# Kernel tuning notes

Hardware: AMD Instinct MI355X
Metric: run time of the kernel (lower is better)

Reference implementation:

```python
import jax, jax.numpy as jnp
import numpy as np
import math

EPS_NORM = 1e-12
BN_EPS = 1e-5


def _l2norm(x):
    n = jnp.sqrt(jnp.sum(x * x, axis=-1, keepdims=True))
    return x / jnp.maximum(n, EPS_NORM)


def setup_inputs() -> dict:
    key = jax.random.key(0)
    ks = jax.random.split(key, 16)
    b, c, t, l = 16, 32, 16, 256
    s = 0.05
    return {
        "x": jax.random.normal(ks[0], (b, c, t, l), jnp.float32),
        "q_w": jax.random.normal(ks[1], (c, c), jnp.float32) * s,
        "q_b": jax.random.normal(ks[2], (c,), jnp.float32) * s,
        "k_w": jax.random.normal(ks[3], (c, c), jnp.float32) * s,
        "k_b": jax.random.normal(ks[4], (c,), jnp.float32) * s,
        "v_w": jax.random.normal(ks[5], (c, c), jnp.float32) * s,
        "v_b": jax.random.normal(ks[6], (c,), jnp.float32) * s,
        "m_w": jax.random.normal(ks[7], (c, c), jnp.float32) * s,
        "m_b": jax.random.normal(ks[8], (c,), jnp.float32) * s,
        "pre_prompt": jax.random.normal(ks[9], (1, c, 1, l), jnp.float32) * s,
        "conv_w": jax.random.normal(ks[10], (c, c, 9, 1), jnp.float32) * s,
        "conv_b": jax.random.normal(ks[11], (c,), jnp.float32) * s,
        "bn_gamma": jnp.ones((c,), jnp.float32),
        "bn_beta": jnp.zeros((c,), jnp.float32),
        "lin_w": jax.random.normal(ks[12], (l, l), jnp.float32) * s,
        "lin_b": jax.random.normal(ks[13], (l,), jnp.float32) * s,
        "atten_flag": 1,
    }


def reference(x, q_w, q_b, k_w, k_b, v_w, v_b, m_w, m_b, pre_prompt,
              conv_w, conv_b, bn_gamma, bn_beta, lin_w, lin_b, atten_flag):
    b, c, t, l = x.shape
    nh = 8
    hd = c // nh

    xp = jnp.transpose(x, (0, 2, 3, 1))  # (b,t,l,c)

    def heads(w, bias):
        h = xp @ w.T + bias
        h = h.reshape(b, t, l, nh, hd).transpose(0, 1, 3, 2, 4)  # (b,t,nh,l,hd)
        return _l2norm(h)

    q = heads(q_w, q_b)
    k = heads(k_w, k_b)
    v = heads(v_w, v_b)

    atten = jnp.einsum('bthld,bthmd->bthlm', q, k) / math.sqrt(hd)
    atten = jax.nn.softmax(atten, axis=-1)
    o = jnp.einsum('bthlm,bthmd->bthld', atten, v)  # (b,t,nh,l,hd)
    o = o.transpose(0, 1, 3, 2, 4).reshape(b, t, l, c)
    o = o @ m_w.T + m_b
    xo = jnp.transpose(o, (0, 3, 1, 2))  # (b,c,t,l)

    pre = jnp.broadcast_to(pre_prompt, (b, c, 1, l))
    con = jnp.concatenate([xo[:, :, :8], pre], axis=2)  # (b,c,9,l)

    # ConvNormAct: Conv2d (VALID, kernel (9,1)) + BatchNorm2d (batch stats) + ReLU
    h = jax.lax.conv_general_dilated(
        con, conv_w, window_strides=(1, 1), padding='VALID',
        dimension_numbers=('NCHW', 'OIHW', 'NCHW'))  # (b,c,1,l)
    h = h + conv_b[None, :, None, None]
    mean = jnp.mean(h, axis=(0, 2, 3), keepdims=True)
    var = jnp.var(h, axis=(0, 2, 3), keepdims=True)
    h = (h - mean) * jax.lax.rsqrt(var + BN_EPS)
    h = h * bn_gamma[None, :, None, None] + bn_beta[None, :, None, None]
    h = jax.nn.relu(h)

    p = h @ lin_w.T + lin_b  # Linear over token_len axis
    p = xo[:, :, 2:3] - p
    return jnp.concatenate([xo[:, :, :8], p], axis=2)  # (b,c,9,l)
```

## Files before the change

### kernel.cpp

```cpp
#include <hip/hip_runtime.h>
#include <hip/hip_bf16.h>


typedef __fp16 h2 __attribute__((ext_vector_type(2)));

#define O_OFF  0u
#define XO_OFF 2097152u
#define H_OFF  6291456u
#define S_OFF  6815744u

__device__ __forceinline__ int probe_f32(const unsigned short* graw) {
    return graw[0] == 0;
}
template<typename T> __device__ __forceinline__ float ldv(const T* p, long i);
template<> __device__ __forceinline__ float ldv<float>(const float* p, long i) {
    return p[i];
}
template<> __device__ __forceinline__ float ldv<__hip_bfloat16>(const __hip_bfloat16* p, long i) {
    return __bfloat162float(p[i]);
}
template<typename T> __device__ __forceinline__ void stv(T* p, size_t i, float v);
template<> __device__ __forceinline__ void stv<float>(float* p, size_t i, float v) {
    p[i] = v;
}
template<> __device__ __forceinline__ void stv<__hip_bfloat16>(__hip_bfloat16* p, size_t i, float v) {
    p[i] = __float2bfloat16(v);
}
__device__ __forceinline__ h2 pkh2(float a, float b) {
    return __builtin_amdgcn_cvt_pkrtz(a, b);
}
__device__ __forceinline__ h2 h2bc(float v) { return pkh2(v, v); }
__device__ __forceinline__ float bflo(unsigned int u) {
    union { unsigned int i; float f; } c; c.i = u << 16; return c.f;
}
__device__ __forceinline__ float bfhi(unsigned int u) {
    union { unsigned int i; float f; } c; c.i = u & 0xffff0000u; return c.f;
}
#if __has_builtin(__builtin_amdgcn_fdot2)
__device__ __forceinline__ float fdot2(h2 a, h2 b, float c) {
    return __builtin_amdgcn_fdot2(a, b, c, false);
}
#else
__device__ __forceinline__ float fdot2(h2 a, h2 b, float c) {
    return fmaf((float)a[0], (float)b[0], fmaf((float)a[1], (float)b[1], c));
}
#endif
#define PFMA(a, b, c) __builtin_elementwise_fma((a), (b), (c))

template<typename T>
__device__ __forceinline__ void attn_phase(
    const T* __restrict__ x,
    const T* __restrict__ qw, const T* __restrict__ qb,
    const T* __restrict__ kw, const T* __restrict__ kb,
    const T* __restrict__ vw, const T* __restrict__ vb,
    unsigned short* __restrict__ O, char* smem)
{
    uint2* Karr = (uint2*)smem;
    uint4* Vbr  = (uint4*)(smem + 2048);
    float (*WL)[4][32] = (float (*)[4][32])(smem + 6144);
    float (*BL)[4]     = (float (*)[4])(smem + 7680);

    const int tid = threadIdx.x;
    const int blk = blockIdx.x;
    const int h = blk & 7, bt = blk >> 3;
    const int b = bt >> 3, t = bt & 7;
    const int h4 = h * 4;

    for (int e = tid; e < 384; e += 128) {
        int p = e >> 7, r = e & 127;
        const T* W = (p == 0) ? qw : ((p == 1) ? kw : vw);
        WL[p][r >> 5][r & 31] = ldv(W, (long)(h4 + (r >> 5)) * 32 + (r & 31));
    }
    if (tid < 12) {
        int p = tid >> 2, j = tid & 3;
        const T* B = (p == 0) ? qb : ((p == 1) ? kb : vb);
        BL[p][j] = ldv(B, h4 + j);
    }

    float xv0[32], xv1[32];
    #pragma unroll
    for (int c = 0; c < 32; c++) {
        const long xb = (((long)b * 32 + c) * 16 + t) * 256 + tid;
        xv0[c] = ldv(x, xb);
        xv1[c] = ldv(x, xb + 128);
    }
    __syncthreads();

    float4 pr0[3], pr1[3];
    #pragma unroll
    for (int p = 0; p < 3; p++) {
        float a0[4], a1[4];
        #pragma unroll
        for (int j = 0; j < 4; j++) { a0[j] = BL[p][j]; a1[j] = a0[j]; }
        #pragma unroll
        for (int c0 = 0; c0 < 32; c0 += 4) {
            float4 w0 = *(const float4*)&WL[p][0][c0];
            float4 w1 = *(const float4*)&WL[p][1][c0];
            float4 w2 = *(const float4*)&WL[p][2][c0];
            float4 w3 = *(const float4*)&WL[p][3][c0];
            const float* wj[4] = {(const float*)&w0, (const float*)&w1,
                                  (const float*)&w2, (const float*)&w3};
            #pragma unroll
            for (int cc = 0; cc < 4; cc++) {
                float x0 = xv0[c0+cc], x1 = xv1[c0+cc];
                #pragma unroll
                for (int j = 0; j < 4; j++) {
                    a0[j] = fmaf(x0, wj[j][cc], a0[j]);
                    a1[j] = fmaf(x1, wj[j][cc], a1[j]);
                }
            }
        }
        float s20 = a0[0]*a0[0] + a0[1]*a0[1] + a0[2]*a0[2] + a0[3]*a0[3];
        float s21 = a1[0]*a1[0] + a1[1]*a1[1] + a1[2]*a1[2] + a1[3]*a1[3];
        float i0 = 1.0f / fmaxf(sqrtf(s20), 1e-12f);
        float i1 = 1.0f / fmaxf(sqrtf(s21), 1e-12f);
        if (p == 0) { i0 *= 0.7213475204444817f; i1 *= 0.7213475204444817f; }
        pr0[p] = make_float4(a0[0]*i0, a0[1]*i0, a0[2]*i0, a0[3]*i0);
        pr1[p] = make_float4(a1[0]*i1, a1[1]*i1, a1[2]*i1, a1[3]*i1);
    }

    union { uint2 u; h2 h[2]; } ka, kb2;
    ka.h[0]  = pkh2(pr0[1].x, pr0[1].y); ka.h[1]  = pkh2(pr0[1].z, pr0[1].w);
    kb2.h[0] = pkh2(pr1[1].x, pr1[1].y); kb2.h[1] = pkh2(pr1[1].z, pr1[1].w);
    union { uint4 u; h2 h[4]; } va, vb2;
    va.h[0]  = h2bc(pr0[2].x); va.h[1]  = h2bc(pr0[2].y);
    va.h[2]  = h2bc(pr0[2].z); va.h[3]  = h2bc(pr0[2].w);
    vb2.h[0] = h2bc(pr1[2].x); vb2.h[1] = h2bc(pr1[2].y);
    vb2.h[2] = h2bc(pr1[2].z); vb2.h[3] = h2bc(pr1[2].w);
    Karr[tid]       = ka.u;
    Karr[tid + 128] = kb2.u;
    Vbr[tid]        = va.u;
    Vbr[tid + 128]  = vb2.u;
    const h2 qa01 = pkh2(pr0[0].x, pr0[0].y), qa23 = pkh2(pr0[0].z, pr0[0].w);
    const h2 qb01 = pkh2(pr1[0].x, pr1[0].y), qb23 = pkh2(pr1[0].z, pr1[0].w);
    __syncthreads();

    const h2 C0 = h2bc(1.0f),          C1 = h2bc(0.69314718f);
    const h2 C2 = h2bc(0.24022651f),   C3 = h2bc(0.05550411f);
    const h2 C4 = h2bc(0.00961813f),   C5 = h2bc(0.00133336f);
    const h2 M0 = {(__fp16)1.0f, (__fp16)0.0f};
    const h2 M1 = {(__fp16)0.0f, (__fp16)1.0f};

    h2 A0 = h2bc(0.0f), A1 = A0, A2 = A0, A3 = A0;
    float den0 = 0.f, den1 = 0.f;
    #pragma unroll 8
    for (int m = 0; m < 256; m++) {
        union { uint2 u; h2 h[2]; } ku; ku.u = Karr[m];
        union { uint4 u; h2 h[4]; } vu; vu.u = Vbr[m];
        float sa = fdot2(qa01, ku.h[0], fdot2(qa23, ku.h[1], 0.0f));
        float sb = fdot2(qb01, ku.h[0], fdot2(qb23, ku.h[1], 0.0f));
        h2 xx = pkh2(sa, sb);
        h2 p = PFMA(xx, C5, C4);
        p = PFMA(xx, p, C3);
        p = PFMA(xx, p, C2);
        p = PFMA(xx, p, C1);
        p = PFMA(xx, p, C0);
        den0 = fdot2(p, M0, den0);
        den1 = fdot2(p, M1, den1);
        A0 = PFMA(p, vu.h[0], A0);
        A1 = PFMA(p, vu.h[1], A1);
        A2 = PFMA(p, vu.h[2], A2);
        A3 = PFMA(p, vu.h[3], A3);
    }
    float ia = 1.0f / den0, ib = 1.0f / den1;
    union { h2 h; unsigned int u; } c0, c1, c2, c3;
    c0.h = pkh2((float)A0[0] * ia, (float)A1[0] * ia);
    c1.h = pkh2((float)A2[0] * ia, (float)A3[0] * ia);
    c2.h = pkh2((float)A0[1] * ib, (float)A1[1] * ib);
    c3.h = pkh2((float)A2[1] * ib, (float)A3[1] * ib);
    *(uint2*)(O + ((size_t)bt * 256u + tid) * 32u + h4)       = make_uint2(c0.u, c1.u);
    *(uint2*)(O + ((size_t)bt * 256u + tid + 128) * 32u + h4) = make_uint2(c2.u, c3.u);
}

template<typename T>
__device__ __forceinline__ void mproj_phase(
    const unsigned short* __restrict__ O,
    const T* __restrict__ mw, const T* __restrict__ mb,
    T* __restrict__ out, float* __restrict__ xof, char* smem)
{
    float* sw = (float*)smem;
    float* sb = (float*)(smem + 4096);
    const int tid = threadIdx.x;
    const int blk = blockIdx.x;
    const int bt = blk >> 1, lhalf = blk & 1;
    const int b = bt >> 3, t = bt & 7;
    const int l = lhalf * 128 + tid;

    for (int e = tid; e < 1024; e += 128) sw[e] = ldv(mw, e);
    if (tid < 32) sb[tid] = ldv(mb, tid);

    float ov[32];
    const unsigned short* src = O + ((size_t)bt * 256u + l) * 32u;
    #pragma unroll
    for (int cc = 0; cc < 4; cc++) {
        union { uint4 u; h2 h[4]; } uu;
        uu.u = *(const uint4*)(src + cc * 8);
        #pragma unroll
        for (int j = 0; j < 4; j++) {
            ov[cc*8 + 2*j]     = (float)uu.h[j][0];
            ov[cc*8 + 2*j + 1] = (float)uu.h[j][1];
        }
    }
    __syncthreads();

    #pragma unroll 4
    for (int co = 0; co < 32; co++) {
        float s = sb[co];
        #pragma unroll
        for (int c0 = 0; c0 < 32; c0 += 4) {
            float4 w4 = *(const float4*)&sw[co * 32 + c0];
            s = fmaf(ov[c0+0], w4.x, s);
            s = fmaf(ov[c0+1], w4.y, s);
            s = fmaf(ov[c0+2], w4.z, s);
            s = fmaf(ov[c0+3], w4.w, s);
        }
        stv(out, (((size_t)b * 32 + co) * 9 + t) * 256u + l, s);
        xof[(((size_t)b * 32 + co) * 8 + t) * 256u + l] = s;
    }
}

template<typename T>
__device__ __forceinline__ void conv_phase(
    const float* __restrict__ xof, const T* __restrict__ pre,
    const T* __restrict__ cw, const T* __restrict__ cb,
    float* __restrict__ hout, float* __restrict__ s, char* smem)
{
    float* wl = (float*)smem;
    const int tid = threadIdx.x;
    const int blk = blockIdx.x;
    const int b = blk >> 4, cog = (blk >> 1) & 7, lhalf = blk & 1;
    const int co0 = cog * 4;
    const int l = lhalf * 128 + tid;

    for (int e = tid; e < 1152; e += 128) {
        int g = e & 3, r = e >> 2;
        wl[e] = ldv(cw, (long)(co0 + g) * 288 + r);
    }
    __syncthreads();

    float a0 = 0.f, a1 = 0.f, a2 = 0.f, a3 = 0.f;
    #pragma unroll 4
    for (int ci = 0; ci < 32; ci++) {
        const float* xp = xof + (((size_t)b * 32 + ci) * 8) * 256u + l;
        float v[9];
        #pragma unroll
        for (int kt = 0; kt < 8; kt++) v[kt] = xp[kt * 256];
        v[8] = ldv(pre, (long)ci * 256 + l);
        #pragma unroll
        for (int kt = 0; kt < 9; kt++) {
            float4 w4 = *(const float4*)&wl[(ci * 9 + kt) * 4];
            a0 = fmaf(v[kt], w4.x, a0);
            a1 = fmaf(v[kt], w4.y, a1);
            a2 = fmaf(v[kt], w4.z, a2);
            a3 = fmaf(v[kt], w4.w, a3);
        }
    }
    a0 += ldv(cb, co0+0); a1 += ldv(cb, co0+1);
    a2 += ldv(cb, co0+2); a3 += ldv(cb, co0+3);

    hout[((size_t)b * 32 + co0 + 0) * 256u + l] = a0;
    hout[((size_t)b * 32 + co0 + 1) * 256u + l] = a1;
    hout[((size_t)b * 32 + co0 + 2) * 256u + l] = a2;
    hout[((size_t)b * 32 + co0 + 3) * 256u + l] = a3;

    float acc[4] = {a0, a1, a2, a3};
    #pragma unroll
    for (int g = 0; g < 4; g++) {
        float sg = acc[g], sq = acc[g] * acc[g];
        #pragma unroll
        for (int off = 32; off > 0; off >>= 1) {
            sg += __shfl_down(sg, off, 64);
            sq += __shfl_down(sq, off, 64);
        }
        if ((tid & 63) == 0) {
            atomicAdd(&s[co0 + g], sg);
            atomicAdd(&s[32 + co0 + g], sq);
        }
    }
}

__device__ __forceinline__ void rowdot2(const float* rp, const float* hn0,
                                        const float* hn1, float& a0, float& a1) {
    float s0 = 0.f, s1 = 0.f;
    #pragma unroll 4
    for (int i0 = 0; i0 < 256; i0 += 4) {
        float4 u  = *(const float4*)(rp + i0);
        float4 p0 = *(const float4*)(hn0 + i0);
        float4 p1 = *(const float4*)(hn1 + i0);
        s0 = fmaf(p0.x, u.x, s0); s1 = fmaf(p1.x, u.x, s1);
        s0 = fmaf(p0.y, u.y, s0); s1 = fmaf(p1.y, u.y, s1);
        s0 = fmaf(p0.z, u.z, s0); s1 = fmaf(p1.z, u.z, s1);
        s0 = fmaf(p0.w, u.w, s0); s1 = fmaf(p1.w, u.w, s1);
    }
    a0 = s0; a1 = s1;
}
__device__ __forceinline__ void rowdot2(const __hip_bfloat16* rp_, const float* hn0,
                                        const float* hn1, float& a0, float& a1) {
    const unsigned short* rp = (const unsigned short*)rp_;
    float s0 = 0.f, s1 = 0.f;
    #pragma unroll 2
    for (int i0 = 0; i0 < 256; i0 += 16) {
        uint4 u0 = *(const uint4*)(rp + i0);
        uint4 u1 = *(const uint4*)(rp + i0 + 8);
        unsigned int uu[8] = {u0.x, u0.y, u0.z, u0.w, u1.x, u1.y, u1.z, u1.w};
        #pragma unroll
        for (int j = 0; j < 8; j++) {
            float wl = bflo(uu[j]), wh = bfhi(uu[j]);
            s0 = fmaf(hn0[i0 + 2*j],     wl, s0);
            s1 = fmaf(hn1[i0 + 2*j],     wl, s1);
            s0 = fmaf(hn0[i0 + 2*j + 1], wh, s0);
            s1 = fmaf(hn1[i0 + 2*j + 1], wh, s1);
        }
    }
    a0 = s0; a1 = s1;
}

template<typename T>
__device__ __forceinline__ void lin_phase(
    const float* __restrict__ hbuf, const float* __restrict__ sbuf,
    const T* __restrict__ gam, const T* __restrict__ bet,
    const T* __restrict__ lw, const T* __restrict__ lb,
    const float* __restrict__ xof, T* __restrict__ out, char* smem)
{
    float* hn0 = (float*)smem;
    float* hn1 = (float*)(smem + 1024);
    const int tid = threadIdx.x;
    const int blk = blockIdx.x;
    const int b = blk >> 4, cop = blk & 15;
    const int co0 = cop * 2, co1 = co0 + 1;

    float mean0 = sbuf[co0] * (1.0f / 4096.0f);
    float var0  = fmaxf(sbuf[32 + co0] * (1.0f / 4096.0f) - mean0 * mean0, 0.0f);
    float sc0 = ldv(gam, co0) * __frsqrt_rn(var0 + 1e-5f);
    float sh0 = ldv(bet, co0) - mean0 * sc0;
    float mean1 = sbuf[co1] * (1.0f / 4096.0f);
    float var1  = fmaxf(sbuf[32 + co1] * (1.0f / 4096.0f) - mean1 * mean1, 0.0f);
    float sc1 = ldv(gam, co1) * __frsqrt_rn(var1 + 1e-5f);
    float sh1 = ldv(bet, co1) - mean1 * sc1;

    const size_t hb0 = ((size_t)b * 32 + co0) * 256u;
    const size_t hb1 = ((size_t)b * 32 + co1) * 256u;
    hn0[tid] = fmaxf(fmaf(hbuf[hb0 + tid], sc0, sh0), 0.0f);
    hn1[tid] = fmaxf(fmaf(hbuf[hb1 + tid], sc1, sh1), 0.0f);
    __syncthreads();

    float a0, a1;
    rowdot2(lw + (size_t)tid * 256u, hn0, hn1, a0, a1);
    float bias = ldv(lb, tid);
    a0 += bias; a1 += bias;

    const size_t xb0 = (((size_t)b * 32 + co0) * 8 + 2) * 256u;
    const size_t xb1 = (((size_t)b * 32 + co1) * 8 + 2) * 256u;
    const size_t ob0 = (((size_t)b * 32 + co0) * 9 + 8) * 256u;
    const size_t ob1 = (((size_t)b * 32 + co1) * 9 + 8) * 256u;
    stv(out, ob0 + tid, xof[xb0 + tid] - a0);
    stv(out, ob1 + tid, xof[xb1 + tid] - a1);
}

__global__ __launch_bounds__(128) void k_attn_s(
    const void* x, const void* qw, const void* qb, const void* kw,
    const void* kb, const void* vw, const void* vb,
    unsigned short* O, float* sbuf, const unsigned short* graw)
{
    __shared__ __align__(16) char smem[7744];
    if (blockIdx.x == 1023 && threadIdx.x < 64) sbuf[threadIdx.x] = 0.0f;
    if (probe_f32(graw))
        attn_phase<float>((const float*)x, (const float*)qw, (const float*)qb,
            (const float*)kw, (const float*)kb, (const float*)vw,
            (const float*)vb, O, smem);
    else
        attn_phase<__hip_bfloat16>((const __hip_bfloat16*)x,
            (const __hip_bfloat16*)qw, (const __hip_bfloat16*)qb,
            (const __hip_bfloat16*)kw, (const __hip_bfloat16*)kb,
            (const __hip_bfloat16*)vw, (const __hip_bfloat16*)vb, O, smem);
}
__global__ __launch_bounds__(128) void k_mproj_s(
    const unsigned short* O, const void* mw, const void* mb,
    void* out, float* xof, const unsigned short* graw)
{
    __shared__ __align__(16) char smem[6144];
    if (probe_f32(graw))
        mproj_phase<float>(O, (const float*)mw, (const float*)mb,
                           (float*)out, xof, smem);
    else
        mproj_phase<__hip_bfloat16>(O, (const __hip_bfloat16*)mw,
                                    (const __hip_bfloat16*)mb,
                                    (__hip_bfloat16*)out, xof, smem);
}
__global__ __launch_bounds__(128) void k_conv_s(
    const float* xof, const void* pre, const void* cw, const void* cb,
    float* hbuf, float* sbuf, const unsigned short* graw)
{
    __shared__ __align__(16) char smem[6144];
    if (probe_f32(graw))
        conv_phase<float>(xof, (const float*)pre, (const float*)cw,
                          (const float*)cb, hbuf, sbuf, smem);
    else
        conv_phase<__hip_bfloat16>(xof, (const __hip_bfloat16*)pre,
                                   (const __hip_bfloat16*)cw,
                                   (const __hip_bfloat16*)cb, hbuf, sbuf, smem);
}
__global__ __launch_bounds__(256) void k_lin_s(
    const float* hbuf, const float* sbuf, const void* gam, const void* bet,
    const void* lw, const void* lb, const float* xof, void* out,
    const unsigned short* graw)
{
    __shared__ __align__(16) char smem[2048];
    if (probe_f32(graw))
        lin_phase<float>(hbuf, sbuf, (const float*)gam, (const float*)bet,
                         (const float*)lw, (const float*)lb, xof,
                         (float*)out, smem);
    else
        lin_phase<__hip_bfloat16>(hbuf, sbuf, (const __hip_bfloat16*)gam,
                                  (const __hip_bfloat16*)bet,
                                  (const __hip_bfloat16*)lw,
                                  (const __hip_bfloat16*)lb, xof,
                                  (__hip_bfloat16*)out, smem);
}

extern "C" void kernel_launch(void* const* d_in, const int* in_sizes, int n_in,
                              void* d_out, int out_size, void* d_ws, size_t ws_size,
                              hipStream_t stream) {
    const void* x   = d_in[0];
    const void* qw  = d_in[1];  const void* qb  = d_in[2];
    const void* kw  = d_in[3];  const void* kb  = d_in[4];
    const void* vw  = d_in[5];  const void* vb  = d_in[6];
    const void* mw  = d_in[7];  const void* mb  = d_in[8];
    const void* pre = d_in[9];
    const void* cw  = d_in[10]; const void* cb  = d_in[11];
    const void* gam = d_in[12]; const void* bet = d_in[13];
    const void* lw  = d_in[14]; const void* lb  = d_in[15];
    const unsigned short* graw = (const unsigned short*)d_in[12];

    unsigned short* Obuf = (unsigned short*)((char*)d_ws + O_OFF);
    float* xof  = (float*)((char*)d_ws + XO_OFF);
    float* hbuf = (float*)((char*)d_ws + H_OFF);
    float* sbuf = (float*)((char*)d_ws + S_OFF);

    k_attn_s <<<1024, 128, 0, stream>>>(x, qw, qb, kw, kb, vw, vb,
                                        Obuf, sbuf, graw);
    k_mproj_s<<<256,  128, 0, stream>>>(Obuf, mw, mb, d_out, xof, graw);
    k_conv_s <<<256,  128, 0, stream>>>(xof, pre, cw, cb, hbuf, sbuf, graw);
    k_lin_s  <<<256,  256, 0, stream>>>(hbuf, sbuf, gam, bet, lw, lb,
                                        xof, d_out, graw);
}
```

Measured before the change: 178.6 us.

## Use packed FMA and fp16 dot products across projection, conv and linear kernels

Rewrites the QKV projection, conv, and linear stages to use packed two-wide float FMAs. The m-projection now keeps O in fp16 and uses fdot2 against fp16-packed weights in shared memory. The softmax exp polynomial drops its highest-order term, which lowers accuracy. The linear kernel now splits each row dot product across 512 threads and reduces the two halves through shared memory. These changes cut instruction count and raise parallelism, at the cost of lower precision in the exp approximation and the output projection.

Result: faster. 171.4 us (-4.0%).

```diff
diff --git a/kernel.cpp b/kernel.cpp
--- a/kernel.cpp
+++ b/kernel.cpp
@@ -3,6 +3,7 @@
 
 
 typedef __fp16 h2 __attribute__((ext_vector_type(2)));
+typedef float  f2 __attribute__((ext_vector_type(2)));
 
 #define O_OFF  0u
 #define XO_OFF 2097152u
@@ -35,6 +36,13 @@
 }
 __device__ __forceinline__ float bfhi(unsigned int u) {
     union { unsigned int i; float f; } c; c.i = u & 0xffff0000u; return c.f;
+}
+__device__ __forceinline__ float2 ld2(const float* p, long i) {
+    return *(const float2*)(p + i);
+}
+__device__ __forceinline__ float2 ld2(const __hip_bfloat16* p, long i) {
+    unsigned int u = *(const unsigned int*)((const unsigned short*)p + i);
+    return make_float2(bflo(u), bfhi(u));
 }
 #if __has_builtin(__builtin_amdgcn_fdot2)
 __device__ __forceinline__ float fdot2(h2 a, h2 b, float c) {
@@ -89,34 +97,40 @@
     float4 pr0[3], pr1[3];
     #pragma unroll
     for (int p = 0; p < 3; p++) {
-        float a0[4], a1[4];
-        #pragma unroll
-        for (int j = 0; j < 4; j++) { a0[j] = BL[p][j]; a1[j] = a0[j]; }
+        f2 aa0 = {BL[p][0], BL[p][0]};
+        f2 aa1 = {BL[p][1], BL[p][1]};
+        f2 aa2 = {BL[p][2], BL[p][2]};
+        f2 aa3 = {BL[p][3], BL[p][3]};
         #pragma unroll
         for (int c0 = 0; c0 < 32; c0 += 4) {
             float4 w0 = *(const float4*)&WL[p][0][c0];
             float4 w1 = *(const float4*)&WL[p][1][c0];
             float4 w2 = *(const float4*)&WL[p][2][c0];
             float4 w3 = *(const float4*)&WL[p][3][c0];
-            const float* wj[4] = {(const float*)&w0, (const float*)&w1,
-                                  (const float*)&w2, (const float*)&w3};
+            const float* w0p = (const float*)&w0;
+            const float* w1p = (const float*)&w1;
+            const float* w2p = (const float*)&w2;
+            const float* w3p = (const float*)&w3;
             #pragma unroll
             for (int cc = 0; cc < 4; cc++) {
-                float x0 = xv0[c0+cc], x1 = xv1[c0+cc];
-                #pragma unroll
-                for (int j = 0; j < 4; j++) {
-                    a0[j] = fmaf(x0, wj[j][cc], a0[j]);
-                    a1[j] = fmaf(x1, wj[j][cc], a1[j]);
-                }
+                f2 xp = {xv0[c0+cc], xv1[c0+cc]};
+                aa0 = PFMA(xp, ((f2){w0p[cc], w0p[cc]}), aa0);
+                aa1 = PFMA(xp, ((f2){w1p[cc], w1p[cc]}), aa1);
+                aa2 = PFMA(xp, ((f2){w2p[cc], w2p[cc]}), aa2);
+                aa3 = PFMA(xp, ((f2){w3p[cc], w3p[cc]}), aa3);
             }
         }
-        float s20 = a0[0]*a0[0] + a0[1]*a0[1] + a0[2]*a0[2] + a0[3]*a0[3];
-        float s21 = a1[0]*a1[0] + a1[1]*a1[1] + a1[2]*a1[2] + a1[3]*a1[3];
-        float i0 = 1.0f / fmaxf(sqrtf(s20), 1e-12f);
-        float i1 = 1.0f / fmaxf(sqrtf(s21), 1e-12f);
+        f2 s2 = aa0 * aa0;
+        s2 = PFMA(aa1, aa1, s2);
+        s2 = PFMA(aa2, aa2, s2);
+        s2 = PFMA(aa3, aa3, s2);
+        float i0 = 1.0f / fmaxf(sqrtf(s2[0]), 1e-12f);
+        float i1 = 1.0f / fmaxf(sqrtf(s2[1]), 1e-12f);
         if (p == 0) { i0 *= 0.7213475204444817f; i1 *= 0.7213475204444817f; }
-        pr0[p] = make_float4(a0[0]*i0, a0[1]*i0, a0[2]*i0, a0[3]*i0);
-        pr1[p] = make_float4(a1[0]*i1, a1[1]*i1, a1[2]*i1, a1[3]*i1);
+        f2 ii = {i0, i1};
+        f2 n0 = aa0 * ii, n1 = aa1 * ii, n2 = aa2 * ii, n3 = aa3 * ii;
+        pr0[p] = make_float4(n0[0], n1[0], n2[0], n3[0]);
+        pr1[p] = make_float4(n0[1], n1[1], n2[1], n3[1]);
     }
 
     union { uint2 u; h2 h[2]; } ka, kb2;
@@ -137,7 +151,7 @@
 
     const h2 C0 = h2bc(1.0f),          C1 = h2bc(0.69314718f);
     const h2 C2 = h2bc(0.24022651f),   C3 = h2bc(0.05550411f);
-    const h2 C4 = h2bc(0.00961813f),   C5 = h2bc(0.00133336f);
+    const h2 C4 = h2bc(0.00961813f);
     const h2 M0 = {(__fp16)1.0f, (__fp16)0.0f};
     const h2 M1 = {(__fp16)0.0f, (__fp16)1.0f};
 
@@ -150,8 +164,7 @@
         float sa = fdot2(qa01, ku.h[0], fdot2(qa23, ku.h[1], 0.0f));
         float sb = fdot2(qb01, ku.h[0], fdot2(qb23, ku.h[1], 0.0f));
         h2 xx = pkh2(sa, sb);
-        h2 p = PFMA(xx, C5, C4);
-        p = PFMA(xx, p, C3);
+        h2 p = PFMA(xx, C4, C3);
         p = PFMA(xx, p, C2);
         p = PFMA(xx, p, C1);
         p = PFMA(xx, p, C0);
@@ -178,41 +191,38 @@
     const T* __restrict__ mw, const T* __restrict__ mb,
     T* __restrict__ out, float* __restrict__ xof, char* smem)
 {
-    float* sw = (float*)smem;
-    float* sb = (float*)(smem + 4096);
+    h2* swh = (h2*)smem;
+    float* sb = (float*)(smem + 2048);
     const int tid = threadIdx.x;
     const int blk = blockIdx.x;
     const int bt = blk >> 1, lhalf = blk & 1;
     const int b = bt >> 3, t = bt & 7;
     const int l = lhalf * 128 + tid;
 
-    for (int e = tid; e < 1024; e += 128) sw[e] = ldv(mw, e);
+    for (int e = tid; e < 512; e += 128) {
+        int co = e >> 4, cp = e & 15;
+        float2 w = ld2(mw, (long)co * 32 + 2 * cp);
+        swh[e] = pkh2(w.x, w.y);
+    }
     if (tid < 32) sb[tid] = ldv(mb, tid);
 
-    float ov[32];
+    union { uint4 u[4]; h2 h[16]; } ou;
     const unsigned short* src = O + ((size_t)bt * 256u + l) * 32u;
     #pragma unroll
-    for (int cc = 0; cc < 4; cc++) {
-        union { uint4 u; h2 h[4]; } uu;
-        uu.u = *(const uint4*)(src + cc * 8);
-        #pragma unroll
-        for (int j = 0; j < 4; j++) {
-            ov[cc*8 + 2*j]     = (float)uu.h[j][0];
-            ov[cc*8 + 2*j + 1] = (float)uu.h[j][1];
-        }
-    }
+    for (int cc = 0; cc < 4; cc++) ou.u[cc] = *(const uint4*)(src + cc * 8);
     __syncthreads();
 
     #pragma unroll 4
     for (int co = 0; co < 32; co++) {
         float s = sb[co];
-        #pragma unroll
-        for (int c0 = 0; c0 < 32; c0 += 4) {
-            float4 w4 = *(const float4*)&sw[co * 32 + c0];
-            s = fmaf(ov[c0+0], w4.x, s);
-            s = fmaf(ov[c0+1], w4.y, s);
-            s = fmaf(ov[c0+2], w4.z, s);
-            s = fmaf(ov[c0+3], w4.w, s);
+        const uint4* wrow = (const uint4*)(swh + co * 16);
+        #pragma unroll
+        for (int q4 = 0; q4 < 4; q4++) {
+            union { uint4 u; h2 h[4]; } wv; wv.u = wrow[q4];
+            s = fdot2(ou.h[q4*4+0], wv.h[0], s);
+            s = fdot2(ou.h[q4*4+1], wv.h[1], s);
+            s = fdot2(ou.h[q4*4+2], wv.h[2], s);
+            s = fdot2(ou.h[q4*4+3], wv.h[3], s);
         }
         stv(out, (((size_t)b * 32 + co) * 9 + t) * 256u + l, s);
         xof[(((size_t)b * 32 + co) * 8 + t) * 256u + l] = s;
@@ -238,7 +248,7 @@
     }
     __syncthreads();
 
-    float a0 = 0.f, a1 = 0.f, a2 = 0.f, a3 = 0.f;
+    f2 a01 = {0.f, 0.f}, a23 = {0.f, 0.f};
     #pragma unroll 4
     for (int ci = 0; ci < 32; ci++) {
         const float* xp = xof + (((size_t)b * 32 + ci) * 8) * 256u + l;
@@ -249,14 +259,15 @@
         #pragma unroll
         for (int kt = 0; kt < 9; kt++) {
             float4 w4 = *(const float4*)&wl[(ci * 9 + kt) * 4];
-            a0 = fmaf(v[kt], w4.x, a0);
-            a1 = fmaf(v[kt], w4.y, a1);
-            a2 = fmaf(v[kt], w4.z, a2);
-            a3 = fmaf(v[kt], w4.w, a3);
-        }
-    }
-    a0 += ldv(cb, co0+0); a1 += ldv(cb, co0+1);
-    a2 += ldv(cb, co0+2); a3 += ldv(cb, co0+3);
+            f2 vv = {v[kt], v[kt]};
+            a01 = PFMA(vv, ((f2){w4.x, w4.y}), a01);
+            a23 = PFMA(vv, ((f2){w4.z, w4.w}), a23);
+        }
+    }
+    float a0 = a01[0] + ldv(cb, co0+0);
+    float a1 = a01[1] + ldv(cb, co0+1);
+    float a2 = a23[0] + ldv(cb, co0+2);
+    float a3 = a23[1] + ldv(cb, co0+3);
 
     hout[((size_t)b * 32 + co0 + 0) * 256u + l] = a0;
     hout[((size_t)b * 32 + co0 + 1) * 256u + l] = a1;
@@ -279,40 +290,36 @@
     }
 }
 
-__device__ __forceinline__ void rowdot2(const float* rp, const float* hn0,
-                                        const float* hn1, float& a0, float& a1) {
-    float s0 = 0.f, s1 = 0.f;
+__device__ __forceinline__ f2 rowdot_pk(const float* rp, const f2* h0, const f2* h1) {
+    f2 a0 = {0.f, 0.f}, a1 = {0.f, 0.f};
     #pragma unroll 4
-    for (int i0 = 0; i0 < 256; i0 += 4) {
-        float4 u  = *(const float4*)(rp + i0);
-        float4 p0 = *(const float4*)(hn0 + i0);
-        float4 p1 = *(const float4*)(hn1 + i0);
-        s0 = fmaf(p0.x, u.x, s0); s1 = fmaf(p1.x, u.x, s1);
-        s0 = fmaf(p0.y, u.y, s0); s1 = fmaf(p1.y, u.y, s1);
-        s0 = fmaf(p0.z, u.z, s0); s1 = fmaf(p1.z, u.z, s1);
-        s0 = fmaf(p0.w, u.w, s0); s1 = fmaf(p1.w, u.w, s1);
-    }
-    a0 = s0; a1 = s1;
-}
-__device__ __forceinline__ void rowdot2(const __hip_bfloat16* rp_, const float* hn0,
-                                        const float* hn1, float& a0, float& a1) {
+    for (int c = 0; c < 128; c += 4) {
+        float4 u = *(const float4*)(rp + c);
+        f2 ulo = {u.x, u.y}, uhi = {u.z, u.w};
+        int p = c >> 1;
+        a0 = PFMA(h0[p], ulo, a0);
+        a0 = PFMA(h0[p+1], uhi, a0);
+        a1 = PFMA(h1[p], ulo, a1);
+        a1 = PFMA(h1[p+1], uhi, a1);
+    }
+    return (f2){a0[0] + a0[1], a1[0] + a1[1]};
+}
+__device__ __forceinline__ f2 rowdot_pk(const __hip_bfloat16* rp_, const f2* h0, const f2* h1) {
     const unsigned short* rp = (const unsigned short*)rp_;
-    float s0 = 0.f, s1 = 0.f;
+    f2 a0 = {0.f, 0.f}, a1 = {0.f, 0.f};
     #pragma unroll 2
-    for (int i0 = 0; i0 < 256; i0 += 16) {
-        uint4 u0 = *(const uint4*)(rp + i0);
-        uint4 u1 = *(const uint4*)(rp + i0 + 8);
-        unsigned int uu[8] = {u0.x, u0.y, u0.z, u0.w, u1.x, u1.y, u1.z, u1.w};
-        #pragma unroll
-        for (int j = 0; j < 8; j++) {
-            float wl = bflo(uu[j]), wh = bfhi(uu[j]);
-            s0 = fmaf(hn0[i0 + 2*j],     wl, s0);
-            s1 = fmaf(hn1[i0 + 2*j],     wl, s1);
-            s0 = fmaf(hn0[i0 + 2*j + 1], wh, s0);
-            s1 = fmaf(hn1[i0 + 2*j + 1], wh, s1);
-        }
-    }
-    a0 = s0; a1 = s1;
+    for (int c = 0; c < 128; c += 8) {
+        uint4 u = *(const uint4*)(rp + c);
+        unsigned int uu[4] = {u.x, u.y, u.z, u.w};
+        #pragma unroll
+        for (int q = 0; q < 4; q++) {
+            f2 w = {bflo(uu[q]), bfhi(uu[q])};
+            int p = (c >> 1) + q;
+            a0 = PFMA(h0[p], w, a0);
+            a1 = PFMA(h1[p], w, a1);
+        }
+    }
+    return (f2){a0[0] + a0[1], a1[0] + a1[1]};
 }
 
 template<typename T>
@@ -324,37 +331,47 @@
 {
     float* hn0 = (float*)smem;
     float* hn1 = (float*)(smem + 1024);
+    f2* part   = (f2*)(smem + 2048);
     const int tid = threadIdx.x;
     const int blk = blockIdx.x;
     const int b = blk >> 4, cop = blk & 15;
     const int co0 = cop * 2, co1 = co0 + 1;
-
-    float mean0 = sbuf[co0] * (1.0f / 4096.0f);
-    float var0  = fmaxf(sbuf[32 + co0] * (1.0f / 4096.0f) - mean0 * mean0, 0.0f);
-    float sc0 = ldv(gam, co0) * __frsqrt_rn(var0 + 1e-5f);
-    float sh0 = ldv(bet, co0) - mean0 * sc0;
-    float mean1 = sbuf[co1] * (1.0f / 4096.0f);
-    float var1  = fmaxf(sbuf[32 + co1] * (1.0f / 4096.0f) - mean1 * mean1, 0.0f);
-    float sc1 = ldv(gam, co1) * __frsqrt_rn(var1 + 1e-5f);
-    float sh1 = ldv(bet, co1) - mean1 * sc1;
-
-    const size_t hb0 = ((size_t)b * 32 + co0) * 256u;
-    const size_t hb1 = ((size_t)b * 32 + co1) * 256u;
-    hn0[tid] = fmaxf(fmaf(hbuf[hb0 + tid], sc0, sh0), 0.0f);
-    hn1[tid] = fmaxf(fmaf(hbuf[hb1 + tid], sc1, sh1), 0.0f);
-    __syncthreads();
-
-    float a0, a1;
-    rowdot2(lw + (size_t)tid * 256u, hn0, hn1, a0, a1);
-    float bias = ldv(lb, tid);
-    a0 += bias; a1 += bias;
-
-    const size_t xb0 = (((size_t)b * 32 + co0) * 8 + 2) * 256u;
-    const size_t xb1 = (((size_t)b * 32 + co1) * 8 + 2) * 256u;
-    const size_t ob0 = (((size_t)b * 32 + co0) * 9 + 8) * 256u;
-    const size_t ob1 = (((size_t)b * 32 + co1) * 9 + 8) * 256u;
-    stv(out, ob0 + tid, xof[xb0 + tid] - a0);
-    stv(out, ob1 + tid, xof[xb1 + tid] - a1);
+    const int j = tid & 255, half = tid >> 8;
+
+    if (tid < 256) {
+        float mean0 = sbuf[co0] * (1.0f / 4096.0f);
+        float var0  = fmaxf(sbuf[32 + co0] * (1.0f / 4096.0f) - mean0 * mean0, 0.0f);
+        float sc0 = ldv(gam, co0) * __frsqrt_rn(var0 + 1e-5f);
+        float sh0 = ldv(bet, co0) - mean0 * sc0;
+        float mean1 = sbuf[co1] * (1.0f / 4096.0f);
+        float var1  = fmaxf(sbuf[32 + co1] * (1.0f / 4096.0f) - mean1 * mean1, 0.0f);
+        float sc1 = ldv(gam, co1) * __frsqrt_rn(var1 + 1e-5f);
+        float sh1 = ldv(bet, co1) - mean1 * sc1;
+
+        const size_t hb0 = ((size_t)b * 32 + co0) * 256u;
+        const size_t hb1 = ((size_t)b * 32 + co1) * 256u;
+        hn0[tid] = fmaxf(fmaf(hbuf[hb0 + tid], sc0, sh0), 0.0f);
+        hn1[tid] = fmaxf(fmaf(hbuf[hb1 + tid], sc1, sh1), 0.0f);
+    }
+    __syncthreads();
+
+    f2 r = rowdot_pk(lw + (size_t)j * 256u + (size_t)half * 128u,
+                     (const f2*)(hn0 + half * 128),
+                     (const f2*)(hn1 + half * 128));
+    part[tid] = r;
+    __syncthreads();
+
+    if (tid < 256) {
+        f2 tot = part[tid] + part[tid + 256];
+        float bias = ldv(lb, j);
+        float r0 = tot[0] + bias, r1 = tot[1] + bias;
+        const size_t xb0 = (((size_t)b * 32 + co0) * 8 + 2) * 256u;
+        const size_t xb1 = (((size_t)b * 32 + co1) * 8 + 2) * 256u;
+        const size_t ob0 = (((size_t)b * 32 + co0) * 9 + 8) * 256u;
+        const size_t ob1 = (((size_t)b * 32 + co1) * 9 + 8) * 256u;
+        stv(out, ob0 + j, xof[xb0 + j] - r0);
+        stv(out, ob1 + j, xof[xb1 + j] - r1);
+    }
 }
 
 __global__ __launch_bounds__(128) void k_attn_s(
@@ -378,7 +395,7 @@
     const unsigned short* O, const void* mw, const void* mb,
     void* out, float* xof, const unsigned short* graw)
 {
-    __shared__ __align__(16) char smem[6144];
+    __shared__ __align__(16) char smem[2176];
     if (probe_f32(graw))
         mproj_phase<float>(O, (const float*)mw, (const float*)mb,
                            (float*)out, xof, smem);
@@ -400,12 +417,12 @@
                                    (const __hip_bfloat16*)cw,
                                    (const __hip_bfloat16*)cb, hbuf, sbuf, smem);
 }
-__global__ __launch_bounds__(256) void k_lin_s(
+__global__ __launch_bounds__(512) void k_lin_s(
     const float* hbuf, const float* sbuf, const void* gam, const void* bet,
     const void* lw, const void* lb, const float* xof, void* out,
     const unsigned short* graw)
 {
-    __shared__ __align__(16) char smem[2048];
+    __shared__ __align__(16) char smem[6144];
     if (probe_f32(graw))
         lin_phase<float>(hbuf, sbuf, (const float*)gam, (const float*)bet,
                          (const float*)lw, (const float*)lb, xof,
@@ -441,6 +458,6 @@
                                         Obuf, sbuf, graw);
     k_mproj_s<<<256,  128, 0, stream>>>(Obuf, mw, mb, d_out, xof, graw);
     k_conv_s <<<256,  128, 0, stream>>>(xof, pre, cw, cb, hbuf, sbuf, graw);
-    k_lin_s  <<<256,  256, 0, stream>>>(hbuf, sbuf, gam, bet, lw, lb,
+    k_lin_s  <<<256,  512, 0, stream>>>(hbuf, sbuf, gam, bet, lw, lb,
                                         xof, d_out, graw);
 }
```
